# Optimization experiments

Measured on AMD Instinct MI355X. Metric: run time of the kernel, lower is better.

Reference implementation:

```python
import jax, jax.numpy as jnp
import numpy as np

EPS = 1e-5


def setup_inputs() -> dict:
    key = jax.random.key(0)
    ks = jax.random.split(key, 4)
    B, C, H, W = 8, 256, 32, 32
    heads, head_dim = 8, 32
    attn_dim = heads * head_dim  # 256
    x = jax.random.normal(ks[0], (B, C, H, W), dtype=jnp.float32)
    gamma = jnp.ones((C,), dtype=jnp.float32)
    beta = jnp.zeros((C,), dtype=jnp.float32)
    w_qkv = jax.random.normal(ks[1], (3 * attn_dim, C), dtype=jnp.float32) * 0.02
    b_qkv = jnp.zeros((3 * attn_dim,), dtype=jnp.float32)
    w_proj = jax.random.normal(ks[2], (C, attn_dim), dtype=jnp.float32) * 0.02
    b_proj = jnp.zeros((C,), dtype=jnp.float32)
    return {"x": x, "gamma": gamma, "beta": beta, "w_qkv": w_qkv,
            "b_qkv": b_qkv, "w_proj": w_proj, "b_proj": b_proj}


def reference(x, gamma, beta, w_qkv, b_qkv, w_proj, b_proj):
    B, C, H, W = x.shape
    heads, head_dim = 8, 32
    scale = head_dim ** -0.5
    N = H * W

    # per-pixel LayerNorm over the channel axis (channels-first)
    mu = jnp.mean(x, axis=1, keepdims=True)
    var = jnp.var(x, axis=1, keepdims=True)
    xn = (x - mu) * jax.lax.rsqrt(var + EPS)
    xn = xn * gamma[None, :, None, None] + beta[None, :, None, None]

    # 1x1 conv QKV == channel matmul: [B, 3*attn_dim, H, W]
    qkv = jnp.einsum('oc,bchw->bohw', w_qkv, xn) + b_qkv[None, :, None, None]
    qkv = qkv.reshape(B, heads, 3 * head_dim, N)
    q, k, v = jnp.split(qkv, 3, axis=2)  # each [B, heads, head_dim, N]

    # attn[b,h,n,m] = sum_d q[b,h,d,n] * k[b,h,d,m]
    attn = jnp.einsum('bhdn,bhdm->bhnm', q, k) * scale
    attn = jax.nn.softmax(attn, axis=-1)

    # out[b,h,d,n] = sum_m v[b,h,d,m] * attn[b,h,n,m]
    out = jnp.einsum('bhdm,bhnm->bhdn', v, attn)
    out = out.reshape(B, heads * head_dim, H, W)

    out = jnp.einsum('oc,bchw->bohw', w_proj, out) + b_proj[None, :, None, None]
    return x + out
```

## Files before the change

kernel.cpp:

```cpp
#include <hip/hip_runtime.h>
#include <hip/hip_bf16.h>

#define BB 8
#define CC 256
#define NPIX 1024
#define NH 8
#define HD 32
#define QKVO 768
#define EPS 1e-5f

typedef __attribute__((ext_vector_type(4)))  float floatx4;
typedef __attribute__((ext_vector_type(16))) float floatx16;
typedef __attribute__((ext_vector_type(8)))  short bf16x8;


__global__ __launch_bounds__(256) void w_prep(const float* __restrict__ wq,
                                              const float* __restrict__ wp,
                                              __hip_bfloat16* __restrict__ wqf,
                                              __hip_bfloat16* __restrict__ wpf) {
    int idx = blockIdx.x * 256 + threadIdx.x;
    const float* src;
    __hip_bfloat16* dst;
    int n;
    if (idx < 24576) { src = wq; dst = wqf; n = idx; }
    else             { src = wp; dst = wpf; n = idx - 24576; }
    const int lane = n & 63, kks = (n >> 6) & 7, tile = n >> 9;
    const int row = tile * 16 + (lane & 15);
    const int col = kks * 32 + (lane >> 4) * 8;
    const float* s = src + (size_t)row * CC + col;
    union { bf16x8 v; __hip_bfloat16 h[8]; } pk;
    #pragma unroll
    for (int j = 0; j < 8; ++j) pk.h[j] = __float2bfloat16(s[j]);
    *(bf16x8*)(dst + (size_t)n * 8) = pk.v;
}

__global__ __launch_bounds__(1024, 8) void ln_qkv(const float* __restrict__ x,
                                                  const float* __restrict__ gamma,
                                                  const float* __restrict__ beta,
                                                  const __hip_bfloat16* __restrict__ wqf,
                                                  const float* __restrict__ bq,
                                                  __hip_bfloat16* __restrict__ qf,
                                                  __hip_bfloat16* __restrict__ kf,
                                                  __hip_bfloat16* __restrict__ vf) {
    __shared__ short xbn[16 * 256];
    __shared__ float s_part[64][17];
    __shared__ float q_part[64][17];
    __shared__ float s_mu[16], s_rs[16];
    __shared__ __hip_bfloat16 qk_stage[64 * 128];

    const int tid  = threadIdx.x;
    const int P0   = blockIdx.x * 16;
    const int b    = P0 >> 10;
    const int nloc = tid & 15;
    const int g    = tid >> 4;
    const float* xb = x + (size_t)b * CC * NPIX + (P0 & 1023);

    float vals[4];
    float s = 0.f, s2 = 0.f;
    #pragma unroll
    for (int j = 0; j < 4; ++j) {
        float v = xb[(size_t)(g * 4 + j) * NPIX + nloc];
        vals[j] = v; s += v; s2 += v * v;
    }
    s_part[g][nloc] = s; q_part[g][nloc] = s2;
    __syncthreads();
    if (tid < 16) {
        float ss = 0.f, qq = 0.f;
        #pragma unroll
        for (int k = 0; k < 64; ++k) { ss += s_part[k][tid]; qq += q_part[k][tid]; }
        float mu  = ss * (1.f / CC);
        float var = qq * (1.f / CC) - mu * mu;
        s_mu[tid] = mu; s_rs[tid] = rsqrtf(var + EPS);
    }
    __syncthreads();

    {
        const float mu = s_mu[nloc], rs = s_rs[nloc];
        union { uint2 u; __hip_bfloat16 h[4]; } pk;
        #pragma unroll
        for (int j = 0; j < 4; ++j) {
            int c = g * 4 + j;
            pk.h[j] = __float2bfloat16((vals[j] - mu) * rs * gamma[c] + beta[c]);
        }
        int idx = (nloc * 256 + g * 4) ^ (nloc << 3);
        *(uint2*)(&xbn[idx]) = pk.u;
    }
    __syncthreads();

    const int w = tid >> 6, lane = tid & 63, lr = lane & 15, lg = lane >> 4;
    const int otb = w * 3;
    floatx4 acc[3] = {};
    for (int kks = 0; kks < 8; ++kks) {
        const int aidx = (lr * 256 + kks * 32 + lg * 8) ^ (lr << 3);
        bf16x8 a = *(const bf16x8*)(&xbn[aidx]);
        #pragma unroll
        for (int nt = 0; nt < 3; ++nt) {
            bf16x8 bfr = *(const bf16x8*)(wqf + (((size_t)(otb + nt) * 8 + kks) * 64 + lane) * 8);
            acc[nt] = __builtin_amdgcn_mfma_f32_16x16x32_bf16(a, bfr, acc[nt], 0, 0, 0);
        }
    }

    const float QSCALE = 0.25503495f;
    const int mb32   = (P0 & 16) + lg * 4;
    const int mloc0  = lg * 4;
    const int tile32 = (P0 & 1023) >> 5;
    #pragma unroll
    for (int nt = 0; nt < 3; ++nt) {
        const int o = (otb + nt) * 16 + lr;
        const int h = o / 96, om = o % 96;
        const float bias = bq[o];
        if (om < 64) {
            const int d = om & 31;
            const bool isq = (om < 32);
            const float sc = isq ? QSCALE : 1.0f;
            const int chunk = (h * 2 + (isq ? 0 : 1)) * 4 + (d >> 3);
            #pragma unroll
            for (int r = 0; r < 4; ++r)
                qk_stage[chunk * 128 + (mloc0 + r) * 8 + (d & 7)] =
                    __float2bfloat16((acc[nt][r] + bias) * sc);
        } else {
            const int d = om - 64;
            const size_t fb = (size_t)((b * NH + h) * 32 + tile32) * 1024;
            const int half = mb32 >> 4, hi2 = (mb32 >> 3) & 1, j0 = mb32 & 7;
            union { unsigned short us[4]; uint2 u; } pv;
            #pragma unroll
            for (int r = 0; r < 4; ++r)
                pv.us[r] = __bfloat16_as_ushort(__float2bfloat16(acc[nt][r] + bias));
            *(uint2*)(vf + fb + half * 512 + (d + 32 * hi2) * 8 + j0) = pv.u;
        }
    }
    __syncthreads();

    {
        const int chunk = tid >> 4;
        const int off   = (tid & 15) * 8;
        const int h     = chunk >> 3;
        const int isK   = (chunk >> 2) & 1;
        const int g3    = chunk & 3;
        const size_t fb = (size_t)((b * NH + h) * 32 + tile32) * 1024;
        __hip_bfloat16* base = (isK ? kf : qf) + fb + g3 * 256 + (size_t)(P0 & 16) * 8;
        *(bf16x8*)(base + off) = *(const bf16x8*)(&qk_stage[chunk * 128 + off]);
    }
}

__global__ __launch_bounds__(1024, 4) void attn_proj(const __hip_bfloat16* __restrict__ qf,
                                                     const __hip_bfloat16* __restrict__ kf,
                                                     const __hip_bfloat16* __restrict__ vf,
                                                     const __hip_bfloat16* __restrict__ wpf,
                                                     const float* __restrict__ bp,
                                                     const float* __restrict__ x,
                                                     float* __restrict__ out) {
    __shared__ __align__(16) char smem_raw[34816 + 16384];
    float (*m_lds)[64][17] = (float (*)[64][17]) smem_raw;
    __hip_bfloat16* o_lds  = (__hip_bfloat16*)(smem_raw + 34816);

    const int bid = blockIdx.x;
    const int b   = bid & 7;
    const int t32 = bid >> 3;
    const int tid = threadIdx.x, w = tid >> 6, lane = tid & 63;
    const int lr = lane & 15, lg = lane >> 4;
    const int lc = lane & 31, hi = lane >> 5;
    const int h  = w >> 1;
    const int mh = w & 1;
    const int bh = b * NH + h;

    const __hip_bfloat16* qb = qf + (size_t)(bh * 32 + t32) * 1024;
    bf16x8 q0 = *(const bf16x8*)(qb + lane * 8);
    bf16x8 q1 = *(const bf16x8*)(qb + 512 + lane * 8);

    const __hip_bfloat16* kb = kf + (size_t)(bh * 32 + mh * 16) * 1024 + lane * 8;
    const __hip_bfloat16* vb = vf + (size_t)(bh * 32 + mh * 16) * 1024 + lane * 8;

    floatx16 oacc = {0.f,0.f,0.f,0.f,0.f,0.f,0.f,0.f,0.f,0.f,0.f,0.f,0.f,0.f,0.f,0.f};
    float ls0 = 0.f, ls1 = 0.f, ls2 = 0.f, ls3 = 0.f;

    #pragma unroll 4
    for (int t = 0; t < 16; ++t) {
        bf16x8 k0 = *(const bf16x8*)(kb + t * 1024);
        bf16x8 k1 = *(const bf16x8*)(kb + t * 1024 + 512);
        bf16x8 v0 = *(const bf16x8*)(vb + t * 1024);
        bf16x8 v1 = *(const bf16x8*)(vb + t * 1024 + 512);

        floatx16 st = {0.f,0.f,0.f,0.f,0.f,0.f,0.f,0.f,0.f,0.f,0.f,0.f,0.f,0.f,0.f,0.f};
        __builtin_amdgcn_s_setprio(1);
        st = __builtin_amdgcn_mfma_f32_32x32x16_bf16(k0, q0, st, 0, 0, 0);
        st = __builtin_amdgcn_mfma_f32_32x32x16_bf16(k1, q1, st, 0, 0, 0);
        __builtin_amdgcn_s_setprio(0);
        float p[16];
        #pragma unroll
        for (int r = 0; r < 16; ++r) p[r] = __builtin_amdgcn_exp2f(st[r]);
        ls0 += p[0] + p[4] + p[8]  + p[12];
        ls1 += p[1] + p[5] + p[9]  + p[13];
        ls2 += p[2] + p[6] + p[10] + p[14];
        ls3 += p[3] + p[7] + p[11] + p[15];
        unsigned int wpk[8];
        #pragma unroll
        for (int k2 = 0; k2 < 8; ++k2)
            asm("v_cvt_pk_bf16_f32 %0, %1, %2" : "=v"(wpk[k2]) : "v"(p[2*k2]), "v"(p[2*k2+1]));
        asm("v_permlane32_swap_b32 %0, %1" : "+v"(wpk[0]), "+v"(wpk[2]));
        asm("v_permlane32_swap_b32 %0, %1" : "+v"(wpk[1]), "+v"(wpk[3]));
        asm("v_permlane32_swap_b32 %0, %1" : "+v"(wpk[4]), "+v"(wpk[6]));
        asm("v_permlane32_swap_b32 %0, %1" : "+v"(wpk[5]), "+v"(wpk[7]));
        union { bf16x8 v; unsigned int u[4]; } pb0, pb1;
        pb0.u[0] = wpk[0]; pb0.u[1] = wpk[1]; pb0.u[2] = wpk[2]; pb0.u[3] = wpk[3];
        pb1.u[0] = wpk[4]; pb1.u[1] = wpk[5]; pb1.u[2] = wpk[6]; pb1.u[3] = wpk[7];
        __builtin_amdgcn_s_setprio(1);
        oacc = __builtin_amdgcn_mfma_f32_32x32x16_bf16(v0, pb0.v, oacc, 0, 0, 0);
        oacc = __builtin_amdgcn_mfma_f32_32x32x16_bf16(v1, pb1.v, oacc, 0, 0, 0);
        __builtin_amdgcn_s_setprio(0);
    }
    float lsum = (ls0 + ls1) + (ls2 + ls3);

    if (mh == 1) {
        #pragma unroll
        for (int r = 0; r < 16; ++r) m_lds[h][lane][r] = oacc[r];
        m_lds[h][lane][16] = lsum;
    }
    __syncthreads();
    if (mh == 0) {
        #pragma unroll
        for (int r = 0; r < 16; ++r) oacc[r] += m_lds[h][lane][r];
        lsum += m_lds[h][lane][16];
        lsum += __shfl_xor(lsum, 32);
        float inv = 1.0f / lsum;
        float (*ts)[33] = (float (*)[33]) &m_lds[h][0][0];
        #pragma unroll
        for (int r = 0; r < 16; ++r) {
            int d = (r & 3) + 8 * (r >> 2) + 4 * hi;
            ts[lc][d] = oacc[r] * inv;
        }
    }
    __syncthreads();
    if (mh == 0) {
        float (*ts)[33] = (float (*)[33]) &m_lds[h][0][0];
        const int q = lane >> 4, nl = lane & 15;
        #pragma unroll
        for (int nt = 0; nt < 2; ++nt) {
            union { __hip_bfloat16 h16[8]; uint4 u4; } ov;
            #pragma unroll
            for (int j = 0; j < 8; ++j)
                ov.h16[j] = __float2bfloat16(ts[nt * 16 + nl][q * 8 + j]);
            *(uint4*)(o_lds + (((size_t)nt * 8 + h) * 64 + lane) * 8) = ov.u4;
        }
    }
    __syncthreads();

    {
        const int ct = w;
        floatx4 acc2[2] = {};
        for (int kks = 0; kks < 8; ++kks) {
            bf16x8 aa = *(const bf16x8*)(wpf + (((size_t)ct * 8 + kks) * 64 + lane) * 8);
            #pragma unroll
            for (int nt = 0; nt < 2; ++nt) {
                bf16x8 bb = *(const bf16x8*)(o_lds + (((size_t)nt * 8 + kks) * 64 + lane) * 8);
                acc2[nt] = __builtin_amdgcn_mfma_f32_16x16x32_bf16(aa, bb, acc2[nt], 0, 0, 0);
            }
        }
        #pragma unroll
        for (int nt = 0; nt < 2; ++nt)
            #pragma unroll
            for (int r = 0; r < 4; ++r) {
                int c = ct * 16 + lg * 4 + r;
                int n = t32 * 32 + nt * 16 + lr;
                size_t idx = ((size_t)b * CC + c) * NPIX + n;
                out[idx] = acc2[nt][r] + bp[c] + x[idx];
            }
    }
}

extern "C" void kernel_launch(void* const* d_in, const int* in_sizes, int n_in,
                              void* d_out, int out_size, void* d_ws, size_t ws_size,
                              hipStream_t stream) {
    const float* x      = (const float*)d_in[0];
    const float* gamma  = (const float*)d_in[1];
    const float* beta   = (const float*)d_in[2];
    const float* w_qkv  = (const float*)d_in[3];
    const float* b_qkv  = (const float*)d_in[4];
    const float* w_proj = (const float*)d_in[5];
    const float* b_proj = (const float*)d_in[6];
    float* out = (float*)d_out;

    char* ws = (char*)d_ws;
    __hip_bfloat16* qfb  = (__hip_bfloat16*)(ws);
    __hip_bfloat16* kfb  = (__hip_bfloat16*)(ws + (4  << 20));
    __hip_bfloat16* vfb  = (__hip_bfloat16*)(ws + (8  << 20));
    __hip_bfloat16* wqf  = (__hip_bfloat16*)(ws + (12 << 20));
    __hip_bfloat16* wpf  = (__hip_bfloat16*)(ws + (12 << 20) + (512 << 10));

    w_prep<<<128, 256, 0, stream>>>(w_qkv, w_proj, wqf, wpf);
    ln_qkv<<<BB * NPIX / 16, 1024, 0, stream>>>(x, gamma, beta, wqf, b_qkv, qfb, kfb, vfb);
    attn_proj<<<BB * 32, 1024, 0, stream>>>(qfb, kfb, vfb, wpf, b_proj, x, out);
}
```

Measured before the change: 43.73 us.

## Use one wave per head in attention, dropping the split-key LDS reduction

The attention kernel now launches 512 threads with one wave per head that loops over all 32 key tiles, instead of two waves each covering half and merging partial sums through LDS. The output projection has each wave compute two channel tiles. The QKV kernel's inner loop also gets an unroll pragma. This removes a barrier and the LDS merge traffic, but it halves the waves per block and doubles the serial attention loop length per wave, with a 256-block grid.

```diff
diff --git a/kernel.cpp b/kernel.cpp
--- a/kernel.cpp
+++ b/kernel.cpp
@@ -90,6 +90,7 @@
     const int w = tid >> 6, lane = tid & 63, lr = lane & 15, lg = lane >> 4;
     const int otb = w * 3;
     floatx4 acc[3] = {};
+    #pragma unroll 2
     for (int kks = 0; kks < 8; ++kks) {
         const int aidx = (lr * 256 + kks * 32 + lg * 8) ^ (lr << 3);
         bf16x8 a = *(const bf16x8*)(&xbn[aidx]);
@@ -143,16 +144,15 @@
     }
 }
 
-__global__ __launch_bounds__(1024, 4) void attn_proj(const __hip_bfloat16* __restrict__ qf,
-                                                     const __hip_bfloat16* __restrict__ kf,
-                                                     const __hip_bfloat16* __restrict__ vf,
-                                                     const __hip_bfloat16* __restrict__ wpf,
-                                                     const float* __restrict__ bp,
-                                                     const float* __restrict__ x,
-                                                     float* __restrict__ out) {
-    __shared__ __align__(16) char smem_raw[34816 + 16384];
-    float (*m_lds)[64][17] = (float (*)[64][17]) smem_raw;
-    __hip_bfloat16* o_lds  = (__hip_bfloat16*)(smem_raw + 34816);
+__global__ __launch_bounds__(512, 6) void attn_proj(const __hip_bfloat16* __restrict__ qf,
+                                                    const __hip_bfloat16* __restrict__ kf,
+                                                    const __hip_bfloat16* __restrict__ vf,
+                                                    const __hip_bfloat16* __restrict__ wpf,
+                                                    const float* __restrict__ bp,
+                                                    const float* __restrict__ x,
+                                                    float* __restrict__ out) {
+    __shared__ float ts_lds[8][32][33];
+    __shared__ __hip_bfloat16 o_lds[2 * 8 * 64 * 8];
 
     const int bid = blockIdx.x;
     const int b   = bid & 7;
@@ -160,22 +160,21 @@
     const int tid = threadIdx.x, w = tid >> 6, lane = tid & 63;
     const int lr = lane & 15, lg = lane >> 4;
     const int lc = lane & 31, hi = lane >> 5;
-    const int h  = w >> 1;
-    const int mh = w & 1;
+    const int h  = w;
     const int bh = b * NH + h;
 
     const __hip_bfloat16* qb = qf + (size_t)(bh * 32 + t32) * 1024;
     bf16x8 q0 = *(const bf16x8*)(qb + lane * 8);
     bf16x8 q1 = *(const bf16x8*)(qb + 512 + lane * 8);
 
-    const __hip_bfloat16* kb = kf + (size_t)(bh * 32 + mh * 16) * 1024 + lane * 8;
-    const __hip_bfloat16* vb = vf + (size_t)(bh * 32 + mh * 16) * 1024 + lane * 8;
+    const __hip_bfloat16* kb = kf + (size_t)(bh * 32) * 1024 + lane * 8;
+    const __hip_bfloat16* vb = vf + (size_t)(bh * 32) * 1024 + lane * 8;
 
     floatx16 oacc = {0.f,0.f,0.f,0.f,0.f,0.f,0.f,0.f,0.f,0.f,0.f,0.f,0.f,0.f,0.f,0.f};
     float ls0 = 0.f, ls1 = 0.f, ls2 = 0.f, ls3 = 0.f;
 
     #pragma unroll 4
-    for (int t = 0; t < 16; ++t) {
+    for (int t = 0; t < 32; ++t) {
         bf16x8 k0 = *(const bf16x8*)(kb + t * 1024);
         bf16x8 k1 = *(const bf16x8*)(kb + t * 1024 + 512);
         bf16x8 v0 = *(const bf16x8*)(vb + t * 1024);
@@ -210,61 +209,51 @@
         __builtin_amdgcn_s_setprio(0);
     }
     float lsum = (ls0 + ls1) + (ls2 + ls3);
-
-    if (mh == 1) {
-        #pragma unroll
-        for (int r = 0; r < 16; ++r) m_lds[h][lane][r] = oacc[r];
-        m_lds[h][lane][16] = lsum;
-    }
-    __syncthreads();
-    if (mh == 0) {
-        #pragma unroll
-        for (int r = 0; r < 16; ++r) oacc[r] += m_lds[h][lane][r];
-        lsum += m_lds[h][lane][16];
-        lsum += __shfl_xor(lsum, 32);
-        float inv = 1.0f / lsum;
-        float (*ts)[33] = (float (*)[33]) &m_lds[h][0][0];
-        #pragma unroll
-        for (int r = 0; r < 16; ++r) {
-            int d = (r & 3) + 8 * (r >> 2) + 4 * hi;
-            ts[lc][d] = oacc[r] * inv;
-        }
-    }
-    __syncthreads();
-    if (mh == 0) {
-        float (*ts)[33] = (float (*)[33]) &m_lds[h][0][0];
+    lsum += __shfl_xor(lsum, 32);
+    const float inv = 1.0f / lsum;
+
+    #pragma unroll
+    for (int r = 0; r < 16; ++r) {
+        int d = (r & 3) + 8 * (r >> 2) + 4 * hi;
+        ts_lds[h][lc][d] = oacc[r] * inv;
+    }
+    {
         const int q = lane >> 4, nl = lane & 15;
         #pragma unroll
         for (int nt = 0; nt < 2; ++nt) {
             union { __hip_bfloat16 h16[8]; uint4 u4; } ov;
             #pragma unroll
             for (int j = 0; j < 8; ++j)
-                ov.h16[j] = __float2bfloat16(ts[nt * 16 + nl][q * 8 + j]);
+                ov.h16[j] = __float2bfloat16(ts_lds[h][nt * 16 + nl][q * 8 + j]);
             *(uint4*)(o_lds + (((size_t)nt * 8 + h) * 64 + lane) * 8) = ov.u4;
         }
     }
     __syncthreads();
 
     {
-        const int ct = w;
-        floatx4 acc2[2] = {};
+        floatx4 acc2[2][2] = {};
         for (int kks = 0; kks < 8; ++kks) {
-            bf16x8 aa = *(const bf16x8*)(wpf + (((size_t)ct * 8 + kks) * 64 + lane) * 8);
-            #pragma unroll
-            for (int nt = 0; nt < 2; ++nt) {
-                bf16x8 bb = *(const bf16x8*)(o_lds + (((size_t)nt * 8 + kks) * 64 + lane) * 8);
-                acc2[nt] = __builtin_amdgcn_mfma_f32_16x16x32_bf16(aa, bb, acc2[nt], 0, 0, 0);
+            bf16x8 bb0 = *(const bf16x8*)(o_lds + (((size_t)0 * 8 + kks) * 64 + lane) * 8);
+            bf16x8 bb1 = *(const bf16x8*)(o_lds + (((size_t)1 * 8 + kks) * 64 + lane) * 8);
+            #pragma unroll
+            for (int c2 = 0; c2 < 2; ++c2) {
+                const int ct = w + c2 * 8;
+                bf16x8 aa = *(const bf16x8*)(wpf + (((size_t)ct * 8 + kks) * 64 + lane) * 8);
+                acc2[c2][0] = __builtin_amdgcn_mfma_f32_16x16x32_bf16(aa, bb0, acc2[c2][0], 0, 0, 0);
+                acc2[c2][1] = __builtin_amdgcn_mfma_f32_16x16x32_bf16(aa, bb1, acc2[c2][1], 0, 0, 0);
             }
         }
         #pragma unroll
-        for (int nt = 0; nt < 2; ++nt)
-            #pragma unroll
-            for (int r = 0; r < 4; ++r) {
-                int c = ct * 16 + lg * 4 + r;
-                int n = t32 * 32 + nt * 16 + lr;
-                size_t idx = ((size_t)b * CC + c) * NPIX + n;
-                out[idx] = acc2[nt][r] + bp[c] + x[idx];
-            }
+        for (int c2 = 0; c2 < 2; ++c2)
+            #pragma unroll
+            for (int nt = 0; nt < 2; ++nt)
+                #pragma unroll
+                for (int r = 0; r < 4; ++r) {
+                    int c = (w + c2 * 8) * 16 + lg * 4 + r;
+                    int n = t32 * 32 + nt * 16 + lr;
+                    size_t idx = ((size_t)b * CC + c) * NPIX + n;
+                    out[idx] = acc2[c2][nt][r] + bp[c] + x[idx];
+                }
     }
 }
 
@@ -289,5 +278,5 @@
 
     w_prep<<<128, 256, 0, stream>>>(w_qkv, w_proj, wqf, wpf);
     ln_qkv<<<BB * NPIX / 16, 1024, 0, stream>>>(x, gamma, beta, wqf, b_qkv, qfb, kfb, vfb);
-    attn_proj<<<BB * 32, 1024, 0, stream>>>(qfb, kfb, vfb, wpf, b_proj, x, out);
-}
+    attn_proj<<<BB * 32, 512, 0, stream>>>(qfb, kfb, vfb, wpf, b_proj, x, out);
+}
```

Result: slower. 45.87 us (+4.9%).
